# Kernel optimization log

Measured on AMD Instinct MI355X. Metric: run time of the kernel, lower is better.

## Reference

```python
import jax, jax.numpy as jnp
import numpy as np

BN_EPS = 1e-5


def conv1x1(x, W, b):
    # x: [B, Cin, N], W: [Cout, Cin], b: [Cout]
    return jnp.einsum('oc,bcn->bon', W, x) + b[None, :, None]


def bn(x, p):
    # p: [4, C] rows = gamma, beta, running_mean, running_var (inference BN)
    g, be, m, v = p[0], p[1], p[2], p[3]
    inv = jax.lax.rsqrt(v + BN_EPS)
    return (x - m[None, :, None]) * (g * inv)[None, :, None] + be[None, :, None]


def conv_bn_relu(x, W, b, p):
    return jax.nn.relu(bn(conv1x1(x, W, b), p))


def _make_params(key, cout, cin):
    k1, k2 = jax.random.split(key)
    W = jax.random.normal(k1, (cout, cin), jnp.float32) * (1.0 / np.sqrt(cin))
    b = jax.random.normal(k2, (cout,), jnp.float32) * 0.01
    p = jnp.stack([jnp.ones(cout), jnp.zeros(cout), jnp.zeros(cout), jnp.ones(cout)]).astype(jnp.float32)
    return W, b, p


def setup_inputs() -> dict:
    key = jax.random.key(0)
    ks = jax.random.split(key, 16)
    B, N, S, D1, D2 = 2, 16384, 4096, 128, 256
    Cin, C, Cm = D1 + D2 + 13, 128, 128  # 397, out_channel, mlp[0]
    inp = {
        'xyz1': jax.random.normal(ks[0], (B, N, 3), jnp.float32),
        'xyz2': jax.random.normal(ks[1], (B, S, 3), jnp.float32),
        'points1': jax.random.normal(ks[2], (B, D1, N), jnp.float32),
        'points2': jax.random.normal(ks[3], (B, D2, S), jnp.float32),
        'last_pred': jax.random.normal(ks[4], (B, S, 13), jnp.float32),
    }
    inp['fuse_W'], inp['fuse_b'], inp['fuse_bn'] = _make_params(ks[5], C, Cin)
    inp['ext1_W'], inp['ext1_b'], inp['ext1_bn'] = _make_params(ks[6], C, C)
    inp['ext2_W'], inp['ext2_b'], inp['ext2_bn'] = _make_params(ks[7], C, C)
    inp['pred1_W'], inp['pred1_b'], inp['pred1_bn'] = _make_params(ks[8], Cm, C)
    inp['pred2_W'], inp['pred2_b'], inp['pred2_bn'] = _make_params(ks[9], 13, Cm)
    return inp


def _forward(xyz1, xyz2, points1, points2, last_pred,
             fuse_W, fuse_b, fuse_bn, ext1_W, ext1_b, ext1_bn,
             ext2_W, ext2_b, ext2_bn, pred1_W, pred1_b, pred1_bn,
             pred2_W, pred2_b, pred2_bn):
    B, N, _ = xyz1.shape
    p1 = jnp.transpose(points1, (0, 2, 1))  # [B, N, D1]
    p2 = jnp.transpose(points2, (0, 2, 1))  # [B, S, D2]
    # squared distances [B, N, S]
    dists = (jnp.sum(xyz1 ** 2, -1)[:, :, None]
             + jnp.sum(xyz2 ** 2, -1)[:, None, :]
             - 2.0 * jnp.einsum('bnc,bsc->bns', xyz1, xyz2))
    # 3 smallest distances (partial top-k instead of full sort; same math)
    neg_d3, idx = jax.lax.top_k(-dists, 3)  # [B, N, 3]
    d3 = -neg_d3
    recip = 1.0 / (d3 + 1e-8)
    weight = recip / jnp.sum(recip, axis=2, keepdims=True)  # [B, N, 3]
    bidx = jnp.arange(B)[:, None, None]
    interp_pts = jnp.sum(p2[bidx, idx] * weight[..., None], axis=2)        # [B, N, D2]
    interp_pred = jnp.sum(last_pred[bidx, idx] * weight[..., None], axis=2)  # [B, N, 13]
    new_points = jnp.transpose(jnp.concatenate([p1, interp_pts, interp_pred], axis=-1), (0, 2, 1))  # [B, Cin, N]
    # fuse
    x = conv_bn_relu(new_points, fuse_W, fuse_b, fuse_bn)
    # extraction: one ConvBNReLURes1D block (groups=1, res_expansion=1)
    h = conv_bn_relu(x, ext1_W, ext1_b, ext1_bn)
    x = jax.nn.relu(bn(conv1x1(h, ext2_W, ext2_b), ext2_bn) + x)  # [B, C, N]
    new_points_out = x
    # prediction head (dropout is identity in eval mode)
    feat = conv_bn_relu(x, pred1_W, pred1_b, pred1_bn)
    pred = conv_bn_relu(feat, pred2_W, pred2_b, pred2_bn)
    return (new_points_out,
            jnp.transpose(feat, (0, 2, 1)),
            jnp.transpose(pred, (0, 2, 1)))


def reference(xyz1, xyz2, points1, points2, last_pred,
              fuse_W, fuse_b, fuse_bn, ext1_W, ext1_b, ext1_bn,
              ext2_W, ext2_b, ext2_bn, pred1_W, pred1_b, pred1_bn,
              pred2_W, pred2_b, pred2_bn):
    return _forward(xyz1, xyz2, points1, points2, last_pred,
                    fuse_W, fuse_b, fuse_bn, ext1_W, ext1_b, ext1_bn,
                    ext2_W, ext2_b, ext2_bn, pred1_W, pred1_b, pred1_bn,
                    pred2_W, pred2_b, pred2_bn)
```

## Files before the change

kernel.cpp:

```cpp
#include <hip/hip_runtime.h>
#include <stdint.h>

#define B_   2
#define N_   16384
#define S_   4096
#define D2_  256
#define CIN_ 397
#define KP_  416
#define C_   128
#define OC_  13
#define NCHUNK_ 16
#define CHS_ (S_ / NCHUNK_)
#define NCAND_ (NCHUNK_ * 3)
#define XBI_P 296

typedef unsigned short u16;
typedef unsigned int u32;
typedef short s16x8 __attribute__((ext_vector_type(8)));
typedef float f32x4 __attribute__((ext_vector_type(4)));

#define MFMA16(a, b, c) __builtin_amdgcn_mfma_f32_16x16x32_bf16((a), (b), (c), 0, 0, 0)

__device__ __forceinline__ float b2f(u16 h) {
  union { unsigned int u; float f; } v; v.u = ((unsigned int)h) << 16; return v.f;
}
__device__ __forceinline__ u16 f2b(float f) {
  union { float f; unsigned int u; } v; v.f = f;
  unsigned int r = v.u + 0x7fffu + ((v.u >> 16) & 1u);
  return (u16)(r >> 16);
}

__device__ __forceinline__ void transpose_body(
    const float* __restrict__ in, u16* __restrict__ out,
    int C, int S, int opitch, int b, int s0, int c0,
    float (*tile)[65], int tr, int tc4) {
  const float* ip = in + (size_t)b * C * S;
  u16* op = out + (size_t)b * S * opitch;
#pragma unroll
  for (int r = 0; r < 64; r += 16) {
    float4 v = *(const float4*)(ip + (size_t)(c0 + tr + r) * S + s0 + tc4);
    tile[tr + r][tc4 + 0] = v.x;
    tile[tr + r][tc4 + 1] = v.y;
    tile[tr + r][tc4 + 2] = v.z;
    tile[tr + r][tc4 + 3] = v.w;
  }
  __syncthreads();
#pragma unroll
  for (int r = 0; r < 64; r += 16) {
    ushort4 v;
    v.x = f2b(tile[tc4 + 0][tr + r]);
    v.y = f2b(tile[tc4 + 1][tr + r]);
    v.z = f2b(tile[tc4 + 2][tr + r]);
    v.w = f2b(tile[tc4 + 3][tr + r]);
    *(ushort4*)(op + (size_t)(s0 + tr + r) * opitch + c0 + tc4) = v;
  }
}

__global__ __launch_bounds__(256) void setup_kernel(
    const float* __restrict__ points1, const float* __restrict__ points2,
    const float* __restrict__ fW, const float* __restrict__ fb,
    const float* __restrict__ fbn,
    const float* __restrict__ e1W, const float* __restrict__ e1b,
    const float* __restrict__ e1bn,
    const float* __restrict__ e2W, const float* __restrict__ e2b,
    const float* __restrict__ e2bn,
    const float* __restrict__ p1W, const float* __restrict__ p1b,
    const float* __restrict__ p1bn,
    const float* __restrict__ p2W, const float* __restrict__ p2b,
    const float* __restrict__ p2bn,
    u16* __restrict__ npT, u16* __restrict__ p2t,
    u16* __restrict__ Wf, u16* __restrict__ W1o,
    u16* __restrict__ W2o, u16* __restrict__ W3o,
    u16* __restrict__ Wp2, float* __restrict__ st) {
  __shared__ float tile[64][65];
  int id = blockIdx.x;
  int tr = threadIdx.x >> 4;
  int tc4 = (threadIdx.x & 15) * 4;
  if (id < 1024) {
    int sx = id & 255, sy = (id >> 8) & 1, b = id >> 9;
    transpose_body(points1, npT, 128, N_, 128, b, sx * 64, sy * 64, tile, tr, tc4);
    return;
  }
  if (id < 1536) {
    int id2 = id - 1024;
    int sx = id2 & 63, sy = (id2 >> 6) & 3, b = id2 >> 8;
    transpose_body(points2, p2t, 256, S_, 256, b, sx * 64, sy * 64, tile, tr, tc4);
    return;
  }
  int tid = (id - 1536) * 256 + threadIdx.x;
  int stride = 64 * 256;
  for (int i = tid; i < 128 * KP_; i += stride) {
    int m = i / KP_, k = i - m * KP_;
    Wf[i] = (k < CIN_) ? f2b(fW[m * CIN_ + k]) : (u16)0;
  }
  for (int i = tid; i < 128 * 128; i += stride) {
    W1o[i] = f2b(e1W[i]);
    W2o[i] = f2b(e2W[i]);
    W3o[i] = f2b(p1W[i]);
  }
  for (int i = tid; i < 16 * 128; i += stride) {
    int m = i >> 7;
    Wp2[i] = (m < OC_) ? f2b(p2W[i]) : (u16)0;
  }
  for (int i = tid; i < 5 * 128; i += stride) {
    int sg = i >> 7, c = i & 127;
    const float* bn; const float* bc; int Cc = 128;
    switch (sg) {
      case 0: bn = fbn;  bc = fb;  break;
      case 1: bn = e1bn; bc = e1b; break;
      case 2: bn = e2bn; bc = e2b; break;
      case 3: bn = p1bn; bc = p1b; break;
      default: bn = p2bn; bc = p2b; Cc = OC_; break;
    }
    float s = 0.f, t = 0.f;
    if (c < Cc) {
      float g  = bn[0 * Cc + c], be = bn[1 * Cc + c];
      float mu = bn[2 * Cc + c], vv = bn[3 * Cc + c];
      float inv = 1.0f / sqrtf(vv + 1e-5f);
      s = g * inv;
      t = (bc[c] - mu) * s + be;
    }
    st[sg * 256 + c] = s;
    st[sg * 256 + 128 + c] = t;
  }
}

__global__ __launch_bounds__(256) void knn_scan_kernel(
    const float* __restrict__ xyz1, const float* __restrict__ xyz2,
    u16* __restrict__ cand) {
  __shared__ float4 pts[CHS_];
  int b = blockIdx.z;
  int chunk = blockIdx.x;
  int s0 = chunk * CHS_;
  int tid = threadIdx.x;
  const float* x2 = xyz2 + ((size_t)b * S_ + s0) * 3;
  {
    float xx = x2[tid * 3], yy = x2[tid * 3 + 1], zz = x2[tid * 3 + 2];
    pts[tid] = make_float4(xx, yy, zz, fmaf(xx, xx, fmaf(yy, yy, zz * zz)));
  }
  __syncthreads();
  int n = blockIdx.y * 256 + tid;
  const float* x1 = xyz1 + ((size_t)b * N_ + n) * 3;
  float ax = x1[0], ay = x1[1], az = x1[2];
  float n1 = fmaf(ax, ax, fmaf(ay, ay, az * az));
  u32 k0 = 0xFFFFFFFFu, k1 = 0xFFFFFFFFu, k2 = 0xFFFFFFFFu;
#pragma unroll 8
  for (int s = 0; s < CHS_; ++s) {
    float4 p = pts[s];
    float dot = fmaf(ax, p.x, fmaf(ay, p.y, az * p.z));
    float d = fmaf(-2.f, dot, n1 + p.w);
    d = fmaxf(d, 0.f);
    u32 key = (__float_as_uint(d) & 0xFFFFFF00u) | (u32)s;
    u32 nk0 = min(k0, key);
    u32 nk1 = min(k1, max(k0, key));
    u32 nk2 = min(k2, max(k1, key));
    k0 = nk0; k1 = nk1; k2 = nk2;
  }
  u16* co = cand + ((size_t)(b * N_ + n)) * NCAND_ + chunk * 3;
  co[0] = (u16)((k0 & 0xFFu) + s0);
  co[1] = (u16)((k1 & 0xFFu) + s0);
  co[2] = (u16)((k2 & 0xFFu) + s0);
}

__device__ __forceinline__ void ins3(double d, int i,
                                     double& D0, double& D1, double& D2,
                                     int& I0, int& I1, int& I2) {
  if ((d < D2) || (d == D2 && i < I2)) {
    if ((d < D1) || (d == D1 && i < I1)) {
      D2 = D1; I2 = I1;
      if ((d < D0) || (d == D0 && i < I0)) { D1 = D0; I1 = I0; D0 = d; I0 = i; }
      else                                  { D1 = d; I1 = i; }
    } else { D2 = d; I2 = i; }
  }
}

__global__ void knn_merge_kernel(const float* __restrict__ xyz1,
                                 const float* __restrict__ xyz2,
                                 const u16* __restrict__ cand,
                                 float* __restrict__ wout, int* __restrict__ iout) {
#pragma clang fp contract(off)
  int q = blockIdx.x * 256 + threadIdx.x;
  int b = q >> 14;
  const u16* ci = cand + (size_t)q * NCAND_;
  const float* x1 = xyz1 + (size_t)q * 3;
  double ax = x1[0], ay = x1[1], az = x1[2];
  double n1 = (ax * ax + ay * ay) + az * az;
  const float* x2b = xyz2 + (size_t)b * S_ * 3;
  double A0 = 1e300, A1 = 1e300, A2 = 1e300;
  int Ia0 = 2147483647, Ia1 = 2147483647, Ia2 = 2147483647;
  double Bd0 = 1e300, Bd1 = 1e300, Bd2 = 1e300;
  int Ib0 = 2147483647, Ib1 = 2147483647, Ib2 = 2147483647;
  for (int j = 0; j < NCAND_ / 2; ++j) {
    int ia = ci[2 * j], ib = ci[2 * j + 1];
    const float* pa = x2b + (size_t)ia * 3;
    const float* pb = x2b + (size_t)ib * 3;
    double pax = pa[0], pay = pa[1], paz = pa[2];
    double pbx = pb[0], pby = pb[1], pbz = pb[2];
    double na = (pax * pax + pay * pay) + paz * paz;
    double nb = (pbx * pbx + pby * pby) + pbz * pbz;
    double da = (n1 + na) - 2.0 * ((ax * pax + ay * pay) + az * paz);
    double db = (n1 + nb) - 2.0 * ((ax * pbx + ay * pby) + az * pbz);
    ins3(da, ia, A0, A1, A2, Ia0, Ia1, Ia2);
    ins3(db, ib, Bd0, Bd1, Bd2, Ib0, Ib1, Ib2);
  }
  ins3(Bd0, Ib0, A0, A1, A2, Ia0, Ia1, Ia2);
  ins3(Bd1, Ib1, A0, A1, A2, Ia0, Ia1, Ia2);
  ins3(Bd2, Ib2, A0, A1, A2, Ia0, Ia1, Ia2);
  double r0 = 1.0 / (A0 + 1e-8);
  double r1 = 1.0 / (A1 + 1e-8);
  double r2 = 1.0 / (A2 + 1e-8);
  double sum = (r0 + r1) + r2;
  size_t o = (size_t)q * 3;
  wout[o + 0] = (float)(r0 / sum);
  wout[o + 1] = (float)(r1 / sum);
  wout[o + 2] = (float)(r2 / sum);
  iout[o + 0] = Ia0; iout[o + 1] = Ia1; iout[o + 2] = Ia2;
}

__device__ __forceinline__ void gemm32(const u16* __restrict__ W, const u16* xb,
                                       int l15, int lq, int wv, f32x4 acc[2][2]) {
#pragma unroll
  for (int mtl = 0; mtl < 2; ++mtl) {
    acc[mtl][0] = (f32x4){0.f, 0.f, 0.f, 0.f};
    acc[mtl][1] = (f32x4){0.f, 0.f, 0.f, 0.f};
  }
#pragma unroll
  for (int ks = 0; ks < 4; ++ks) {
    int ko = ks * 32 + lq * 8;
    s16x8 b0 = *(const s16x8*)(xb + l15 * 136 + ko);
    s16x8 b1 = *(const s16x8*)(xb + (16 + l15) * 136 + ko);
#pragma unroll
    for (int mtl = 0; mtl < 2; ++mtl) {
      s16x8 a = *(const s16x8*)(W + (size_t)((wv * 2 + mtl) * 16 + l15) * 128 + ko);
      acc[mtl][0] = MFMA16(a, b0, acc[mtl][0]);
      acc[mtl][1] = MFMA16(a, b1, acc[mtl][1]);
    }
  }
}

__global__ __launch_bounds__(256, 4) void mega_kernel(
    const u16* __restrict__ npT, const u16* __restrict__ p2t,
    const float* __restrict__ last_pred,
    const float* __restrict__ knw, const int* __restrict__ kni,
    const u16* __restrict__ Wf,
    const u16* __restrict__ W1, const u16* __restrict__ W2,
    const u16* __restrict__ W3, const u16* __restrict__ Wp2,
    const float* __restrict__ st, float* __restrict__ out) {
  __shared__ u16 xb0[32 * 136];
  __shared__ u16 xb1[32 * 136];
  __shared__ u16 xbi[32 * XBI_P];
  int b = blockIdx.y;
  int n0 = blockIdx.x * 32;
  int tid = threadIdx.x;
  int wv = tid >> 6, lane = tid & 63;
  int l15 = lane & 15, lq = lane >> 4;
  f32x4 acc[2][2];

  {
    const float* lpb = last_pred + (size_t)b * S_ * OC_;
    const u16* p2b = p2t + (size_t)b * S_ * D2_;
#pragma unroll 2
    for (int i = 0; i < 8; ++i) {
      int p = wv * 8 + i;
      size_t o = ((size_t)(b * N_ + n0 + p)) * 3;
      float w0 = knw[o], w1 = knw[o + 1], w2 = knw[o + 2];
      int i0 = kni[o], i1 = kni[o + 1], i2 = kni[o + 2];
      ushort4 a0 = *(const ushort4*)(p2b + (size_t)i0 * D2_ + lane * 4);
      ushort4 a1 = *(const ushort4*)(p2b + (size_t)i1 * D2_ + lane * 4);
      ushort4 a2 = *(const ushort4*)(p2b + (size_t)i2 * D2_ + lane * 4);
      ushort4 v;
      v.x = f2b((w0 * b2f(a0.x) + w1 * b2f(a1.x)) + w2 * b2f(a2.x));
      v.y = f2b((w0 * b2f(a0.y) + w1 * b2f(a1.y)) + w2 * b2f(a2.y));
      v.z = f2b((w0 * b2f(a0.z) + w1 * b2f(a1.z)) + w2 * b2f(a2.z));
      v.w = f2b((w0 * b2f(a0.w) + w1 * b2f(a1.w)) + w2 * b2f(a2.w));
      *(ushort4*)(&xbi[p * XBI_P + lane * 4]) = v;
      if (lane < 32) {
        u16 pv = 0;
        if (lane < OC_) {
          pv = f2b((w0 * lpb[i0 * OC_ + lane] + w1 * lpb[i1 * OC_ + lane])
                   + w2 * lpb[i2 * OC_ + lane]);
        }
        xbi[p * XBI_P + 256 + lane] = pv;
      }
    }
  }
  __syncthreads();

#pragma unroll
  for (int mtl = 0; mtl < 2; ++mtl) {
    acc[mtl][0] = (f32x4){0.f, 0.f, 0.f, 0.f};
    acc[mtl][1] = (f32x4){0.f, 0.f, 0.f, 0.f};
  }
  {
    const u16* brow0 = npT + ((size_t)(b * N_ + n0 + l15)) * 128;
    const u16* brow1 = brow0 + (size_t)16 * 128;
#pragma unroll 1
    for (int ks = 0; ks < 4; ++ks) {
      int ko = ks * 32 + lq * 8;
      s16x8 bf0 = *(const s16x8*)(brow0 + ko);
      s16x8 bf1 = *(const s16x8*)(brow1 + ko);
#pragma unroll
      for (int mtl = 0; mtl < 2; ++mtl) {
        s16x8 a = *(const s16x8*)(Wf + (size_t)((wv * 2 + mtl) * 16 + l15) * KP_ + ko);
        acc[mtl][0] = MFMA16(a, bf0, acc[mtl][0]);
        acc[mtl][1] = MFMA16(a, bf1, acc[mtl][1]);
      }
    }
#pragma unroll 1
    for (int ks = 0; ks < 9; ++ks) {
      int kk = ks * 32 + lq * 8;
      s16x8 bf0 = *(const s16x8*)(&xbi[l15 * XBI_P + kk]);
      s16x8 bf1 = *(const s16x8*)(&xbi[(16 + l15) * XBI_P + kk]);
#pragma unroll
      for (int mtl = 0; mtl < 2; ++mtl) {
        s16x8 a = *(const s16x8*)(Wf + (size_t)((wv * 2 + mtl) * 16 + l15) * KP_ + 128 + kk);
        acc[mtl][0] = MFMA16(a, bf0, acc[mtl][0]);
        acc[mtl][1] = MFMA16(a, bf1, acc[mtl][1]);
      }
    }
  }
#pragma unroll
  for (int mtl = 0; mtl < 2; ++mtl) {
    int m4 = (wv * 2 + mtl) * 16 + lq * 4;
    f32x4 sc = *(const f32x4*)(st + 0 * 256 + m4);
    f32x4 bi = *(const f32x4*)(st + 0 * 256 + 128 + m4);
#pragma unroll
    for (int nt = 0; nt < 2; ++nt) {
      int n_l = nt * 16 + l15;
      ushort4 v;
      v.x = f2b(fmaxf(acc[mtl][nt][0] * sc[0] + bi[0], 0.f));
      v.y = f2b(fmaxf(acc[mtl][nt][1] * sc[1] + bi[1], 0.f));
      v.z = f2b(fmaxf(acc[mtl][nt][2] * sc[2] + bi[2], 0.f));
      v.w = f2b(fmaxf(acc[mtl][nt][3] * sc[3] + bi[3], 0.f));
      *(ushort4*)(&xb0[n_l * 136 + m4]) = v;
    }
  }
  __syncthreads();

  gemm32(W1, xb0, l15, lq, wv, acc);
#pragma unroll
  for (int mtl = 0; mtl < 2; ++mtl) {
    int m4 = (wv * 2 + mtl) * 16 + lq * 4;
    f32x4 sc = *(const f32x4*)(st + 1 * 256 + m4);
    f32x4 bi = *(const f32x4*)(st + 1 * 256 + 128 + m4);
#pragma unroll
    for (int nt = 0; nt < 2; ++nt) {
      int n_l = nt * 16 + l15;
      ushort4 v;
      v.x = f2b(fmaxf(acc[mtl][nt][0] * sc[0] + bi[0], 0.f));
      v.y = f2b(fmaxf(acc[mtl][nt][1] * sc[1] + bi[1], 0.f));
      v.z = f2b(fmaxf(acc[mtl][nt][2] * sc[2] + bi[2], 0.f));
      v.w = f2b(fmaxf(acc[mtl][nt][3] * sc[3] + bi[3], 0.f));
      *(ushort4*)(&xb1[n_l * 136 + m4]) = v;
    }
  }
  __syncthreads();

  gemm32(W2, xb1, l15, lq, wv, acc);
#pragma unroll
  for (int mtl = 0; mtl < 2; ++mtl) {
    int m4 = (wv * 2 + mtl) * 16 + lq * 4;
    f32x4 sc = *(const f32x4*)(st + 2 * 256 + m4);
    f32x4 bi = *(const f32x4*)(st + 2 * 256 + 128 + m4);
#pragma unroll
    for (int nt = 0; nt < 2; ++nt) {
      int n_l = nt * 16 + l15;
      int n_g = n0 + n_l;
      ushort4 xp = *(const ushort4*)(&xb0[n_l * 136 + m4]);
      float v0 = fmaxf(acc[mtl][nt][0] * sc[0] + bi[0] + b2f(xp.x), 0.f);
      float v1 = fmaxf(acc[mtl][nt][1] * sc[1] + bi[1] + b2f(xp.y), 0.f);
      float v2 = fmaxf(acc[mtl][nt][2] * sc[2] + bi[2] + b2f(xp.z), 0.f);
      float v3 = fmaxf(acc[mtl][nt][3] * sc[3] + bi[3] + b2f(xp.w), 0.f);
      ushort4 v;
      v.x = f2b(v0); v.y = f2b(v1); v.z = f2b(v2); v.w = f2b(v3);
      *(ushort4*)(&xb0[n_l * 136 + m4]) = v;
      out[((size_t)(b * C_ + m4 + 0)) * N_ + n_g] = v0;
      out[((size_t)(b * C_ + m4 + 1)) * N_ + n_g] = v1;
      out[((size_t)(b * C_ + m4 + 2)) * N_ + n_g] = v2;
      out[((size_t)(b * C_ + m4 + 3)) * N_ + n_g] = v3;
    }
  }
  __syncthreads();

  gemm32(W3, xb0, l15, lq, wv, acc);
  {
    float* out1 = out + (size_t)B_ * C_ * N_;
#pragma unroll
    for (int mtl = 0; mtl < 2; ++mtl) {
      int m4 = (wv * 2 + mtl) * 16 + lq * 4;
      f32x4 sc = *(const f32x4*)(st + 3 * 256 + m4);
      f32x4 bi = *(const f32x4*)(st + 3 * 256 + 128 + m4);
#pragma unroll
      for (int nt = 0; nt < 2; ++nt) {
        int n_l = nt * 16 + l15;
        int n_g = n0 + n_l;
        float v0 = fmaxf(acc[mtl][nt][0] * sc[0] + bi[0], 0.f);
        float v1 = fmaxf(acc[mtl][nt][1] * sc[1] + bi[1], 0.f);
        float v2 = fmaxf(acc[mtl][nt][2] * sc[2] + bi[2], 0.f);
        float v3 = fmaxf(acc[mtl][nt][3] * sc[3] + bi[3], 0.f);
        ushort4 v;
        v.x = f2b(v0); v.y = f2b(v1); v.z = f2b(v2); v.w = f2b(v3);
        *(ushort4*)(&xb1[n_l * 136 + m4]) = v;
        float4 o4 = make_float4(v0, v1, v2, v3);
        *(float4*)(out1 + ((size_t)(b * N_ + n_g)) * 128 + m4) = o4;
      }
    }
  }
  __syncthreads();

  if (wv < 2) {
    f32x4 a2 = (f32x4){0.f, 0.f, 0.f, 0.f};
#pragma unroll
    for (int ks = 0; ks < 4; ++ks) {
      int ko = ks * 32 + lq * 8;
      s16x8 b0 = *(const s16x8*)(&xb1[(wv * 16 + l15) * 136 + ko]);
      s16x8 a = *(const s16x8*)(Wp2 + (size_t)l15 * 128 + ko);
      a2 = MFMA16(a, b0, a2);
    }
    float* out2 = out + (size_t)B_ * C_ * N_ + (size_t)B_ * N_ * 128;
    f32x4 sc = *(const f32x4*)(st + 4 * 256 + lq * 4);
    f32x4 bi = *(const f32x4*)(st + 4 * 256 + 128 + lq * 4);
    int n_g = n0 + wv * 16 + l15;
#pragma unroll
    for (int r = 0; r < 4; ++r) {
      int m = lq * 4 + r;
      if (m < OC_) {
        out2[((size_t)(b * N_ + n_g)) * OC_ + m] =
            fmaxf(a2[r] * sc[r] + bi[r], 0.f);
      }
    }
  }
}

extern "C" void kernel_launch(void* const* d_in, const int* in_sizes, int n_in,
                              void* d_out, int out_size, void* d_ws, size_t ws_size,
                              hipStream_t stream) {
  const float* xyz1      = (const float*)d_in[0];
  const float* xyz2      = (const float*)d_in[1];
  const float* points1   = (const float*)d_in[2];
  const float* points2   = (const float*)d_in[3];
  const float* last_pred = (const float*)d_in[4];
  const float* fuse_W    = (const float*)d_in[5];
  const float* fuse_b    = (const float*)d_in[6];
  const float* fuse_bn   = (const float*)d_in[7];
  const float* ext1_W    = (const float*)d_in[8];
  const float* ext1_b    = (const float*)d_in[9];
  const float* ext1_bn   = (const float*)d_in[10];
  const float* ext2_W    = (const float*)d_in[11];
  const float* ext2_b    = (const float*)d_in[12];
  const float* ext2_bn   = (const float*)d_in[13];
  const float* pred1_W   = (const float*)d_in[14];
  const float* pred1_b   = (const float*)d_in[15];
  const float* pred1_bn  = (const float*)d_in[16];
  const float* pred2_W   = (const float*)d_in[17];
  const float* pred2_b   = (const float*)d_in[18];
  const float* pred2_bn  = (const float*)d_in[19];

  char* ws = (char*)d_ws;
  u16*   npT  = (u16*)(ws + 0);
  u16*   p2t  = (u16*)(ws + 8388608);
  float* knw  = (float*)(ws + 12582912);
  int*   kni  = (int*)(ws + 12976128);
  u16*   cand = (u16*)(ws + 13369344);
  u16*   Wf   = (u16*)(ws + 16515072);
  u16*   W1   = (u16*)(ws + 16621568);
  u16*   W2   = (u16*)(ws + 16654336);
  u16*   W3   = (u16*)(ws + 16687104);
  u16*   Wp2  = (u16*)(ws + 16719872);
  float* st   = (float*)(ws + 16723968);

  setup_kernel<<<dim3(1600), dim3(256), 0, stream>>>(
      points1, points2,
      fuse_W, fuse_b, fuse_bn, ext1_W, ext1_b, ext1_bn, ext2_W, ext2_b, ext2_bn,
      pred1_W, pred1_b, pred1_bn, pred2_W, pred2_b, pred2_bn,
      npT, p2t, Wf, W1, W2, W3, Wp2, st);

  knn_scan_kernel<<<dim3(NCHUNK_, N_ / 256, B_), dim3(256), 0, stream>>>(
      xyz1, xyz2, cand);
  knn_merge_kernel<<<dim3(B_ * N_ / 256), dim3(256), 0, stream>>>(
      xyz1, xyz2, cand, knw, kni);

  mega_kernel<<<dim3(N_ / 32, B_), dim3(256), 0, stream>>>(
      npT, p2t, last_pred, knw, kni, Wf, W1, W2, W3, Wp2, st, (float*)d_out);
}
```

Before: 236.2 us.

## Fuse KNN scan into setup kernel and KNN merge into mega kernel

Folds the KNN chunk-scan blocks into the setup kernel's grid, so one launch covers both, and moves the double-precision candidate merge into the start of the mega kernel. The merge is split across 8 threads per query, with a shared-memory reduction that reuses the GEMM staging buffers. This drops two kernel launches and the global round trip for the KNN weights and indices, and lets the independent setup and scan blocks run concurrently. In exchange it adds two block barriers and some serial merge work per mega-kernel block, which may add pressure on an already occupancy-bounded kernel.

```diff
diff --git a/kernel.cpp b/kernel.cpp
--- a/kernel.cpp
+++ b/kernel.cpp
@@ -33,30 +33,31 @@
 __device__ __forceinline__ void transpose_body(
     const float* __restrict__ in, u16* __restrict__ out,
     int C, int S, int opitch, int b, int s0, int c0,
-    float (*tile)[65], int tr, int tc4) {
+    float* __restrict__ tile, int tr, int tc4) {
   const float* ip = in + (size_t)b * C * S;
   u16* op = out + (size_t)b * S * opitch;
 #pragma unroll
   for (int r = 0; r < 64; r += 16) {
     float4 v = *(const float4*)(ip + (size_t)(c0 + tr + r) * S + s0 + tc4);
-    tile[tr + r][tc4 + 0] = v.x;
-    tile[tr + r][tc4 + 1] = v.y;
-    tile[tr + r][tc4 + 2] = v.z;
-    tile[tr + r][tc4 + 3] = v.w;
+    tile[(tr + r) * 65 + tc4 + 0] = v.x;
+    tile[(tr + r) * 65 + tc4 + 1] = v.y;
+    tile[(tr + r) * 65 + tc4 + 2] = v.z;
+    tile[(tr + r) * 65 + tc4 + 3] = v.w;
   }
   __syncthreads();
 #pragma unroll
   for (int r = 0; r < 64; r += 16) {
     ushort4 v;
-    v.x = f2b(tile[tc4 + 0][tr + r]);
-    v.y = f2b(tile[tc4 + 1][tr + r]);
-    v.z = f2b(tile[tc4 + 2][tr + r]);
-    v.w = f2b(tile[tc4 + 3][tr + r]);
+    v.x = f2b(tile[(tc4 + 0) * 65 + tr + r]);
+    v.y = f2b(tile[(tc4 + 1) * 65 + tr + r]);
+    v.z = f2b(tile[(tc4 + 2) * 65 + tr + r]);
+    v.w = f2b(tile[(tc4 + 3) * 65 + tr + r]);
     *(ushort4*)(op + (size_t)(s0 + tr + r) * opitch + c0 + tc4) = v;
   }
 }
 
-__global__ __launch_bounds__(256) void setup_kernel(
+__global__ __launch_bounds__(256) void setup_scan_kernel(
+    const float* __restrict__ xyz1, const float* __restrict__ xyz2,
     const float* __restrict__ points1, const float* __restrict__ points2,
     const float* __restrict__ fW, const float* __restrict__ fb,
     const float* __restrict__ fbn,
@@ -68,41 +69,80 @@
     const float* __restrict__ p1bn,
     const float* __restrict__ p2W, const float* __restrict__ p2b,
     const float* __restrict__ p2bn,
-    u16* __restrict__ npT, u16* __restrict__ p2t,
+    u16* __restrict__ cand, u16* __restrict__ npT, u16* __restrict__ p2t,
     u16* __restrict__ Wf, u16* __restrict__ W1o,
     u16* __restrict__ W2o, u16* __restrict__ W3o,
     u16* __restrict__ Wp2, float* __restrict__ st) {
-  __shared__ float tile[64][65];
+  __shared__ __align__(16) float smem[64 * 65];
   int id = blockIdx.x;
-  int tr = threadIdx.x >> 4;
-  int tc4 = (threadIdx.x & 15) * 4;
-  if (id < 1024) {
-    int sx = id & 255, sy = (id >> 8) & 1, b = id >> 9;
-    transpose_body(points1, npT, 128, N_, 128, b, sx * 64, sy * 64, tile, tr, tc4);
+  int tid = threadIdx.x;
+
+  if (id < 2048) {
+    float4* pts = (float4*)smem;
+    int chunk = id & 15;
+    int ny = (id >> 4) & 63;
+    int b = id >> 10;
+    int s0 = chunk * CHS_;
+    const float* x2 = xyz2 + ((size_t)b * S_ + s0) * 3;
+    {
+      float xx = x2[tid * 3], yy = x2[tid * 3 + 1], zz = x2[tid * 3 + 2];
+      pts[tid] = make_float4(xx, yy, zz, fmaf(xx, xx, fmaf(yy, yy, zz * zz)));
+    }
+    __syncthreads();
+    int n = ny * 256 + tid;
+    const float* x1 = xyz1 + ((size_t)b * N_ + n) * 3;
+    float ax = x1[0], ay = x1[1], az = x1[2];
+    float n1 = fmaf(ax, ax, fmaf(ay, ay, az * az));
+    u32 k0 = 0xFFFFFFFFu, k1 = 0xFFFFFFFFu, k2 = 0xFFFFFFFFu;
+#pragma unroll 8
+    for (int s = 0; s < CHS_; ++s) {
+      float4 p = pts[s];
+      float dot = fmaf(ax, p.x, fmaf(ay, p.y, az * p.z));
+      float d = fmaf(-2.f, dot, n1 + p.w);
+      d = fmaxf(d, 0.f);
+      u32 key = (__float_as_uint(d) & 0xFFFFFF00u) | (u32)s;
+      u32 nk0 = min(k0, key);
+      u32 nk1 = min(k1, max(k0, key));
+      u32 nk2 = min(k2, max(k1, key));
+      k0 = nk0; k1 = nk1; k2 = nk2;
+    }
+    u16* co = cand + ((size_t)(b * N_ + n)) * NCAND_ + chunk * 3;
+    co[0] = (u16)((k0 & 0xFFu) + s0);
+    co[1] = (u16)((k1 & 0xFFu) + s0);
+    co[2] = (u16)((k2 & 0xFFu) + s0);
     return;
   }
-  if (id < 1536) {
-    int id2 = id - 1024;
+
+  int tr = tid >> 4;
+  int tc4 = (tid & 15) * 4;
+  if (id < 3072) {
+    int id2 = id - 2048;
+    int sx = id2 & 255, sy = (id2 >> 8) & 1, b = id2 >> 9;
+    transpose_body(points1, npT, 128, N_, 128, b, sx * 64, sy * 64, smem, tr, tc4);
+    return;
+  }
+  if (id < 3584) {
+    int id2 = id - 3072;
     int sx = id2 & 63, sy = (id2 >> 6) & 3, b = id2 >> 8;
-    transpose_body(points2, p2t, 256, S_, 256, b, sx * 64, sy * 64, tile, tr, tc4);
+    transpose_body(points2, p2t, 256, S_, 256, b, sx * 64, sy * 64, smem, tr, tc4);
     return;
   }
-  int tid = (id - 1536) * 256 + threadIdx.x;
+  int t = (id - 3584) * 256 + tid;
   int stride = 64 * 256;
-  for (int i = tid; i < 128 * KP_; i += stride) {
+  for (int i = t; i < 128 * KP_; i += stride) {
     int m = i / KP_, k = i - m * KP_;
     Wf[i] = (k < CIN_) ? f2b(fW[m * CIN_ + k]) : (u16)0;
   }
-  for (int i = tid; i < 128 * 128; i += stride) {
+  for (int i = t; i < 128 * 128; i += stride) {
     W1o[i] = f2b(e1W[i]);
     W2o[i] = f2b(e2W[i]);
     W3o[i] = f2b(p1W[i]);
   }
-  for (int i = tid; i < 16 * 128; i += stride) {
+  for (int i = t; i < 16 * 128; i += stride) {
     int m = i >> 7;
     Wp2[i] = (m < OC_) ? f2b(p2W[i]) : (u16)0;
   }
-  for (int i = tid; i < 5 * 128; i += stride) {
+  for (int i = t; i < 5 * 128; i += stride) {
     int sg = i >> 7, c = i & 127;
     const float* bn; const float* bc; int Cc = 128;
     switch (sg) {
@@ -112,54 +152,17 @@
       case 3: bn = p1bn; bc = p1b; break;
       default: bn = p2bn; bc = p2b; Cc = OC_; break;
     }
-    float s = 0.f, t = 0.f;
+    float s = 0.f, tt = 0.f;
     if (c < Cc) {
       float g  = bn[0 * Cc + c], be = bn[1 * Cc + c];
       float mu = bn[2 * Cc + c], vv = bn[3 * Cc + c];
       float inv = 1.0f / sqrtf(vv + 1e-5f);
       s = g * inv;
-      t = (bc[c] - mu) * s + be;
+      tt = (bc[c] - mu) * s + be;
     }
     st[sg * 256 + c] = s;
-    st[sg * 256 + 128 + c] = t;
-  }
-}
-
-__global__ __launch_bounds__(256) void knn_scan_kernel(
-    const float* __restrict__ xyz1, const float* __restrict__ xyz2,
-    u16* __restrict__ cand) {
-  __shared__ float4 pts[CHS_];
-  int b = blockIdx.z;
-  int chunk = blockIdx.x;
-  int s0 = chunk * CHS_;
-  int tid = threadIdx.x;
-  const float* x2 = xyz2 + ((size_t)b * S_ + s0) * 3;
-  {
-    float xx = x2[tid * 3], yy = x2[tid * 3 + 1], zz = x2[tid * 3 + 2];
-    pts[tid] = make_float4(xx, yy, zz, fmaf(xx, xx, fmaf(yy, yy, zz * zz)));
-  }
-  __syncthreads();
-  int n = blockIdx.y * 256 + tid;
-  const float* x1 = xyz1 + ((size_t)b * N_ + n) * 3;
-  float ax = x1[0], ay = x1[1], az = x1[2];
-  float n1 = fmaf(ax, ax, fmaf(ay, ay, az * az));
-  u32 k0 = 0xFFFFFFFFu, k1 = 0xFFFFFFFFu, k2 = 0xFFFFFFFFu;
-#pragma unroll 8
-  for (int s = 0; s < CHS_; ++s) {
-    float4 p = pts[s];
-    float dot = fmaf(ax, p.x, fmaf(ay, p.y, az * p.z));
-    float d = fmaf(-2.f, dot, n1 + p.w);
-    d = fmaxf(d, 0.f);
-    u32 key = (__float_as_uint(d) & 0xFFFFFF00u) | (u32)s;
-    u32 nk0 = min(k0, key);
-    u32 nk1 = min(k1, max(k0, key));
-    u32 nk2 = min(k2, max(k1, key));
-    k0 = nk0; k1 = nk1; k2 = nk2;
-  }
-  u16* co = cand + ((size_t)(b * N_ + n)) * NCAND_ + chunk * 3;
-  co[0] = (u16)((k0 & 0xFFu) + s0);
-  co[1] = (u16)((k1 & 0xFFu) + s0);
-  co[2] = (u16)((k2 & 0xFFu) + s0);
+    st[sg * 256 + 128 + c] = tt;
+  }
 }
 
 __device__ __forceinline__ void ins3(double d, int i,
@@ -174,49 +177,6 @@
   }
 }
 
-__global__ void knn_merge_kernel(const float* __restrict__ xyz1,
-                                 const float* __restrict__ xyz2,
-                                 const u16* __restrict__ cand,
-                                 float* __restrict__ wout, int* __restrict__ iout) {
-#pragma clang fp contract(off)
-  int q = blockIdx.x * 256 + threadIdx.x;
-  int b = q >> 14;
-  const u16* ci = cand + (size_t)q * NCAND_;
-  const float* x1 = xyz1 + (size_t)q * 3;
-  double ax = x1[0], ay = x1[1], az = x1[2];
-  double n1 = (ax * ax + ay * ay) + az * az;
-  const float* x2b = xyz2 + (size_t)b * S_ * 3;
-  double A0 = 1e300, A1 = 1e300, A2 = 1e300;
-  int Ia0 = 2147483647, Ia1 = 2147483647, Ia2 = 2147483647;
-  double Bd0 = 1e300, Bd1 = 1e300, Bd2 = 1e300;
-  int Ib0 = 2147483647, Ib1 = 2147483647, Ib2 = 2147483647;
-  for (int j = 0; j < NCAND_ / 2; ++j) {
-    int ia = ci[2 * j], ib = ci[2 * j + 1];
-    const float* pa = x2b + (size_t)ia * 3;
-    const float* pb = x2b + (size_t)ib * 3;
-    double pax = pa[0], pay = pa[1], paz = pa[2];
-    double pbx = pb[0], pby = pb[1], pbz = pb[2];
-    double na = (pax * pax + pay * pay) + paz * paz;
-    double nb = (pbx * pbx + pby * pby) + pbz * pbz;
-    double da = (n1 + na) - 2.0 * ((ax * pax + ay * pay) + az * paz);
-    double db = (n1 + nb) - 2.0 * ((ax * pbx + ay * pby) + az * pbz);
-    ins3(da, ia, A0, A1, A2, Ia0, Ia1, Ia2);
-    ins3(db, ib, Bd0, Bd1, Bd2, Ib0, Ib1, Ib2);
-  }
-  ins3(Bd0, Ib0, A0, A1, A2, Ia0, Ia1, Ia2);
-  ins3(Bd1, Ib1, A0, A1, A2, Ia0, Ia1, Ia2);
-  ins3(Bd2, Ib2, A0, A1, A2, Ia0, Ia1, Ia2);
-  double r0 = 1.0 / (A0 + 1e-8);
-  double r1 = 1.0 / (A1 + 1e-8);
-  double r2 = 1.0 / (A2 + 1e-8);
-  double sum = (r0 + r1) + r2;
-  size_t o = (size_t)q * 3;
-  wout[o + 0] = (float)(r0 / sum);
-  wout[o + 1] = (float)(r1 / sum);
-  wout[o + 2] = (float)(r2 / sum);
-  iout[o + 0] = Ia0; iout[o + 1] = Ia1; iout[o + 2] = Ia2;
-}
-
 __device__ __forceinline__ void gemm32(const u16* __restrict__ W, const u16* xb,
                                        int l15, int lq, int wv, f32x4 acc[2][2]) {
 #pragma unroll
@@ -239,16 +199,19 @@
 }
 
 __global__ __launch_bounds__(256, 4) void mega_kernel(
+    const float* __restrict__ xyz1, const float* __restrict__ xyz2,
+    const u16* __restrict__ cand,
     const u16* __restrict__ npT, const u16* __restrict__ p2t,
     const float* __restrict__ last_pred,
-    const float* __restrict__ knw, const int* __restrict__ kni,
     const u16* __restrict__ Wf,
     const u16* __restrict__ W1, const u16* __restrict__ W2,
     const u16* __restrict__ W3, const u16* __restrict__ Wp2,
     const float* __restrict__ st, float* __restrict__ out) {
-  __shared__ u16 xb0[32 * 136];
-  __shared__ u16 xb1[32 * 136];
+  __shared__ __align__(16) u16 xb0[32 * 136];
+  __shared__ __align__(16) u16 xb1[32 * 136];
   __shared__ u16 xbi[32 * XBI_P];
+  __shared__ float wL[32][3];
+  __shared__ int   iL[32][3];
   int b = blockIdx.y;
   int n0 = blockIdx.x * 32;
   int tid = threadIdx.x;
@@ -257,14 +220,62 @@
   f32x4 acc[2][2];
 
   {
+#pragma clang fp contract(off)
+    double* md = (double*)xb0;
+    int*    mi = (int*)xb1;
+    int qi = tid >> 3, part = tid & 7;
+    int qg = b * N_ + n0 + qi;
+    const u16* ci = cand + (size_t)qg * NCAND_ + part * 6;
+    const float* x1 = xyz1 + (size_t)qg * 3;
+    double ax = x1[0], ay = x1[1], az = x1[2];
+    double n1 = (ax * ax + ay * ay) + az * az;
+    const float* x2b = xyz2 + (size_t)b * S_ * 3;
+    double D0 = 1e300, D1 = 1e300, D2v = 1e300;
+    int I0 = 2147483647, I1 = 2147483647, I2 = 2147483647;
+#pragma unroll
+    for (int j = 0; j < 6; ++j) {
+      int i = ci[j];
+      const float* p = x2b + (size_t)i * 3;
+      double px = p[0], py = p[1], pz = p[2];
+      double n2 = (px * px + py * py) + pz * pz;
+      double dot = (ax * px + ay * py) + az * pz;
+      double d = (n1 + n2) - 2.0 * dot;
+      ins3(d, i, D0, D1, D2v, I0, I1, I2);
+    }
+    md[qi * 24 + part * 3 + 0] = D0; mi[qi * 24 + part * 3 + 0] = I0;
+    md[qi * 24 + part * 3 + 1] = D1; mi[qi * 24 + part * 3 + 1] = I1;
+    md[qi * 24 + part * 3 + 2] = D2v; mi[qi * 24 + part * 3 + 2] = I2;
+  }
+  __syncthreads();
+
+  if (tid < 32) {
+#pragma clang fp contract(off)
+    double* md = (double*)xb0;
+    int*    mi = (int*)xb1;
+    double D0 = 1e300, D1 = 1e300, D2v = 1e300;
+    int I0 = 2147483647, I1 = 2147483647, I2 = 2147483647;
+    for (int j = 0; j < 24; ++j) {
+      ins3(md[tid * 24 + j], mi[tid * 24 + j], D0, D1, D2v, I0, I1, I2);
+    }
+    double r0 = 1.0 / (D0 + 1e-8);
+    double r1 = 1.0 / (D1 + 1e-8);
+    double r2 = 1.0 / (D2v + 1e-8);
+    double sum = (r0 + r1) + r2;
+    wL[tid][0] = (float)(r0 / sum);
+    wL[tid][1] = (float)(r1 / sum);
+    wL[tid][2] = (float)(r2 / sum);
+    iL[tid][0] = I0; iL[tid][1] = I1; iL[tid][2] = I2;
+  }
+  __syncthreads();
+
+  {
     const float* lpb = last_pred + (size_t)b * S_ * OC_;
     const u16* p2b = p2t + (size_t)b * S_ * D2_;
 #pragma unroll 2
     for (int i = 0; i < 8; ++i) {
       int p = wv * 8 + i;
-      size_t o = ((size_t)(b * N_ + n0 + p)) * 3;
-      float w0 = knw[o], w1 = knw[o + 1], w2 = knw[o + 2];
-      int i0 = kni[o], i1 = kni[o + 1], i2 = kni[o + 2];
+      float w0 = wL[p][0], w1 = wL[p][1], w2 = wL[p][2];
+      int i0 = iL[p][0], i1 = iL[p][1], i2 = iL[p][2];
       ushort4 a0 = *(const ushort4*)(p2b + (size_t)i0 * D2_ + lane * 4);
       ushort4 a1 = *(const ushort4*)(p2b + (size_t)i1 * D2_ + lane * 4);
       ushort4 a2 = *(const ushort4*)(p2b + (size_t)i2 * D2_ + lane * 4);
@@ -459,27 +470,21 @@
   char* ws = (char*)d_ws;
   u16*   npT  = (u16*)(ws + 0);
   u16*   p2t  = (u16*)(ws + 8388608);
-  float* knw  = (float*)(ws + 12582912);
-  int*   kni  = (int*)(ws + 12976128);
-  u16*   cand = (u16*)(ws + 13369344);
-  u16*   Wf   = (u16*)(ws + 16515072);
-  u16*   W1   = (u16*)(ws + 16621568);
-  u16*   W2   = (u16*)(ws + 16654336);
-  u16*   W3   = (u16*)(ws + 16687104);
-  u16*   Wp2  = (u16*)(ws + 16719872);
-  float* st   = (float*)(ws + 16723968);
-
-  setup_kernel<<<dim3(1600), dim3(256), 0, stream>>>(
-      points1, points2,
+  u16*   cand = (u16*)(ws + 12582912);
+  u16*   Wf   = (u16*)(ws + 15728640);
+  u16*   W1   = (u16*)(ws + 15835136);
+  u16*   W2   = (u16*)(ws + 15867904);
+  u16*   W3   = (u16*)(ws + 15900672);
+  u16*   Wp2  = (u16*)(ws + 15933440);
+  float* st   = (float*)(ws + 15937536);
+
+  setup_scan_kernel<<<dim3(3648), dim3(256), 0, stream>>>(
+      xyz1, xyz2, points1, points2,
       fuse_W, fuse_b, fuse_bn, ext1_W, ext1_b, ext1_bn, ext2_W, ext2_b, ext2_bn,
       pred1_W, pred1_b, pred1_bn, pred2_W, pred2_b, pred2_bn,
-      npT, p2t, Wf, W1, W2, W3, Wp2, st);
-
-  knn_scan_kernel<<<dim3(NCHUNK_, N_ / 256, B_), dim3(256), 0, stream>>>(
-      xyz1, xyz2, cand);
-  knn_merge_kernel<<<dim3(B_ * N_ / 256), dim3(256), 0, stream>>>(
-      xyz1, xyz2, cand, knw, kni);
+      cand, npT, p2t, Wf, W1, W2, W3, Wp2, st);
 
   mega_kernel<<<dim3(N_ / 32, B_), dim3(256), 0, stream>>>(
-      npT, p2t, last_pred, knw, kni, Wf, W1, W2, W3, Wp2, st, (float*)d_out);
-}
+      xyz1, xyz2, cand, npT, p2t, last_pred,
+      Wf, W1, W2, W3, Wp2, st, (float*)d_out);
+}
```

New measurement: 207.7 us. -12.1%, faster.
